# Kernel tuning notes

Hardware: AMD Instinct MI355X
Metric: run time of the kernel (lower is better)

The kernel has to match this reference:

```python
import jax, jax.numpy as jnp
import numpy as np

N_USERS = 100000
N_ITEMS = 50000
N = N_USERS + N_ITEMS
EMB_DIM = 64
N_LAYERS = 3
NNZ = 6400000
BATCH = 4096


def setup_inputs() -> dict:
    key = jax.random.key(0)
    k = jax.random.split(key, 7)
    user_emb = 0.1 * jax.random.normal(k[0], (N_USERS, EMB_DIM), dtype=jnp.float32)
    item_emb = 0.1 * jax.random.normal(k[1], (N_ITEMS, EMB_DIM), dtype=jnp.float32)
    graph_val = jax.random.uniform(k[2], (NNZ,), dtype=jnp.float32) * 0.05
    graph_src = jax.random.randint(k[3], (NNZ,), 0, N, dtype=jnp.int64) if jax.config.jax_enable_x64 else jax.random.randint(k[3], (NNZ,), 0, N).astype(jnp.int32)
    graph_dst = jax.random.randint(k[4], (NNZ,), 0, N).astype(graph_src.dtype)
    users = jax.random.randint(k[5], (BATCH,), 0, N_USERS).astype(graph_src.dtype)
    items = jax.random.randint(k[6], (BATCH,), 0, N_ITEMS).astype(graph_src.dtype)
    return {"user_emb": user_emb, "item_emb": item_emb, "graph_val": graph_val,
            "graph_src": graph_src, "graph_dst": graph_dst, "users": users, "items": items}


def _spmm(val, src, dst, x):
    # y[src] += val * x[dst]  -- sparse (COO) matrix @ dense
    return jax.ops.segment_sum(val[:, None] * x[dst], src, num_segments=N)


def reference(user_emb, item_emb, graph_val, graph_src, graph_dst, users, items):
    all_emb = jnp.concatenate([user_emb, item_emb], axis=0)  # [N, d]
    acc = all_emb  # running sum over layers (fused mean accumulation)
    x = all_emb
    for _ in range(N_LAYERS):
        x = _spmm(graph_val, graph_src, graph_dst, x)
        acc = acc + x
    light_out = acc / (N_LAYERS + 1)
    all_users = light_out[:N_USERS]
    all_items = light_out[N_USERS:]
    scores = jnp.sum(all_users[users] * all_items[items], axis=1)  # [B]
    return scores
```

## Files before the change

### kernel.cpp

```cpp
#include <hip/hip_runtime.h>


constexpr int N_USERS = 100000;
constexpr int N_ITEMS = 50000;
constexpr int N_NODES = N_USERS + N_ITEMS;
constexpr int EMB = 64;
constexpr int NNZ = 6400000;
constexpr int BATCH = 4096;

constexpr int BSHIFT = 9;
constexpr int BWIDTH = 1 << BSHIFT;
constexpr int NB = (N_NODES + BWIDTH - 1) >> BSHIFT;
constexpr int NBPAD = 512;
constexpr int BSTRIDE = 23500;
constexpr int PBSTRIDE = 26624;

constexpr int TILE = 5120;
constexpr int P1_BLOCKS = NNZ / TILE;
constexpr int EPT1 = TILE / 256;
constexpr int IQ_BLOCKS = (N_NODES * 8 + 255) / 256;
constexpr int GI_BLOCKS = (BATCH * 2 * 64) / 256;
constexpr int SBLOCKS  = (N_NODES * 8 + 255) / 256;
constexpr int SELBLOCKS = (BATCH * 2 * 8) / 256;

constexpr float QSCALE = 327680.0f;
constexpr float QINV   = 1.0f / 327680.0f;

__device__ __forceinline__ int   ntl_i32(const int* p)   { return __builtin_nontemporal_load(p); }
__device__ __forceinline__ float ntl_f32(const float* p) { return __builtin_nontemporal_load(p); }

__global__ void gcur_init_kernel(int* __restrict__ gcur) {
    int i = blockIdx.x * blockDim.x + threadIdx.x;
    if (i < NB) gcur[i] = i * BSTRIDE;
}

__device__ __forceinline__ float ubf0(unsigned x) { return (float)(x & 0xffu); }
__device__ __forceinline__ float ubf1(unsigned x) { return (float)((x >> 8) & 0xffu); }
__device__ __forceinline__ float ubf2(unsigned x) { return (float)((x >> 16) & 0xffu); }
__device__ __forceinline__ float ubf3(unsigned x) { return (float)(x >> 24); }

__global__ void fused_build_kernel(const int* __restrict__ src, const int* __restrict__ dst,
                                   const float* __restrict__ val, int* __restrict__ gcur,
                                   unsigned* __restrict__ sx, unsigned short* __restrict__ srow,
                                   const float* __restrict__ ue, const float* __restrict__ ie,
                                   const int* __restrict__ users, const int* __restrict__ items,
                                   unsigned char* __restrict__ x8, float* __restrict__ scl,
                                   float* __restrict__ accb) {
    int bx = blockIdx.x;
    int t = threadIdx.x;
    if (bx < P1_BLOCKS) {
        __shared__ int hist[NBPAD];
        __shared__ int gbase[NBPAD];
        __shared__ int cur[NBPAD];
        __shared__ int sbuf[NBPAD];
        __shared__ int lbase[NBPAD];
        __shared__ uint2 ebuf[TILE];
        int tile = bx * TILE;
        int srcs[EPT1];
        #pragma unroll
        for (int k = 0; k < EPT1; ++k) srcs[k] = ntl_i32(src + tile + t + k * 256);
        for (int i = t; i < NBPAD; i += 256) { hist[i] = 0; cur[i] = 0; }
        __syncthreads();
        #pragma unroll
        for (int k = 0; k < EPT1; ++k) atomicAdd(&hist[srcs[k] >> BSHIFT], 1);
        __syncthreads();
        for (int i = t; i < NB; i += 256) {
            int h = hist[i];
            gbase[i] = (h > 0) ? atomicAdd(&gcur[i], h) : 0;
        }
        for (int i = t; i < NBPAD; i += 256) sbuf[i] = hist[i];
        __syncthreads();
        int* pin = sbuf; int* pout = lbase;
        for (int off = 1; off < NBPAD; off <<= 1) {
            for (int i = t; i < NBPAD; i += 256) {
                int v = pin[i];
                if (i >= off) v += pin[i - off];
                pout[i] = v;
            }
            __syncthreads();
            int* tmp = pin; pin = pout; pout = tmp;
        }
        for (int i = t; i < NBPAD; i += 256) lbase[i] = pin[i] - hist[i];
        __syncthreads();
        #pragma unroll
        for (int k = 0; k < EPT1; ++k) {
            int i = tile + t + k * 256;
            int s = srcs[k];
            int b = s >> BSHIFT;
            int c = atomicAdd(&cur[b], 1);
            int d = ntl_i32(dst + i);
            float v = ntl_f32(val + i);
            unsigned q = (unsigned)(v * QSCALE);
            if (q > 16383u) q = 16383u;
            ebuf[lbase[b] + c] = make_uint2((q << 18) | (unsigned)d, (unsigned)s);
        }
        __syncthreads();
        #pragma unroll
        for (int k = 0; k < EPT1; ++k) {
            int j = t + k * 256;
            uint2 e = ebuf[j];
            int b = (int)(e.y >> BSHIFT);
            unsigned pos = (unsigned)(gbase[b] + (j - lbase[b]));
            if (pos < (unsigned)((b + 1) * BSTRIDE)) {
                sx[pos] = e.x;
                srow[pos] = (unsigned short)(e.y & (BWIDTH - 1));
            }
        }
        return;
    }
    bx -= P1_BLOCKS;
    if (bx < IQ_BLOCKS) {
        int gid = bx * 256 + t;
        int row = gid >> 3;
        if (row >= N_NODES) return;
        int l8 = t & 7;
        const float* srcp = (row < N_USERS) ? (ue + (size_t)row * EMB)
                                            : (ie + (size_t)(row - N_USERS) * EMB);
        const float4* p = (const float4*)(srcp + l8 * 8);
        float4 f0 = p[0], f1 = p[1];
        float v[8] = {f0.x, f0.y, f0.z, f0.w, f1.x, f1.y, f1.z, f1.w};
        float m = 0.f;
        #pragma unroll
        for (int k = 0; k < 8; ++k) m = fmaxf(m, fabsf(v[k]));
        m = fmaxf(m, __shfl_xor(m, 1, 64));
        m = fmaxf(m, __shfl_xor(m, 2, 64));
        m = fmaxf(m, __shfl_xor(m, 4, 64));
        float inv = (m > 0.f) ? 127.f / m : 0.f;
        unsigned w0 = 0, w1 = 0;
        #pragma unroll
        for (int k = 0; k < 4; ++k)
            w0 |= (((unsigned)((int)rintf(v[k] * inv) + 128)) & 0xffu) << (8 * k);
        #pragma unroll
        for (int k = 0; k < 4; ++k)
            w1 |= (((unsigned)((int)rintf(v[4 + k] * inv) + 128)) & 0xffu) << (8 * k);
        *(uint2*)(x8 + (((size_t)row) << 6) + l8 * 8) = make_uint2(w0, w1);
        if (l8 == 0) scl[row] = m * (1.f / 127.f);
        return;
    }
    bx -= IQ_BLOCKS;
    {
        int gid = bx * 256 + t;
        int w = gid >> 6;
        int lane = t & 63;
        if (w >= BATCH * 2) return;
        int b = w >> 1;
        float v;
        if (w & 1) v = ie[(long long)items[b] * EMB + lane];
        else       v = ue[(long long)users[b] * EMB + lane];
        accb[(long long)w * EMB + lane] = v;
    }
}

__global__ void p2_sort_kernel(const int* __restrict__ gcur,
                               const unsigned* __restrict__ sx,
                               const unsigned short* __restrict__ srow,
                               unsigned* __restrict__ epack, unsigned* __restrict__ prow) {
    __shared__ int hist[BWIDTH], sA[BWIDTH], sB[BWIDTH], cur[BWIDTH];
    int b = blockIdx.x;
    int t = threadIdx.x;
    int cnt = gcur[b] - b * BSTRIDE;
    if (cnt > BSTRIDE) cnt = BSTRIDE;
    if (cnt < 0) cnt = 0;
    int sbase = b * BSTRIDE;
    hist[t] = 0;
    __syncthreads();
    for (int j = t; j < cnt; j += 512)
        atomicAdd(&hist[srow[sbase + j]], 1);
    __syncthreads();
    sA[t] = (hist[t] + 7) >> 3;
    __syncthreads();
    int* pin = sA; int* pout = sB;
    for (int off = 1; off < BWIDTH; off <<= 1) {
        int v = pin[t];
        if (t >= off) v += pin[t - off];
        pout[t] = v;
        __syncthreads();
        int* tmp = pin; pin = pout; pout = tmp;
    }
    {
        int c = hist[t];
        int pw = (c + 7) >> 3;
        int ps = pin[t] - pw;
        unsigned poff = (unsigned)(b * PBSTRIDE + 8 * ps);
        int fit = (PBSTRIDE - 8 * ps) >> 3;
        if (fit < 0) fit = 0;
        if (pw > fit) pw = fit;
        if (pw > 15) pw = 15;
        cur[t] = (int)poff;
        int node = (b << BSHIFT) + t;
        if (node < N_NODES) prow[node] = (poff << 4) | (unsigned)pw;
        for (int s = c; s < 8 * pw; ++s) epack[poff + s] = 0;
    }
    __syncthreads();
    unsigned bend = (unsigned)((b + 1) * PBSTRIDE);
    for (int j = t; j < cnt; j += 512) {
        int row = (int)srow[sbase + j];
        unsigned ex = sx[sbase + j];
        int p = atomicAdd(&cur[row], 1);
        if ((unsigned)p < bend) epack[p] = ex;
    }
}

__device__ __forceinline__ void row_gather_q8(unsigned pr, int lane,
                                              const unsigned* __restrict__ epack,
                                              const unsigned char* __restrict__ x8,
                                              const float* __restrict__ scl,
                                              float acc[8]) {
    const int l8 = lane & 7;
    const int qb = lane & 56;
    const unsigned li8 = (unsigned)l8 * 8u;
    float a0 = 0, a1 = 0, a2 = 0, a3 = 0, a4 = 0, a5 = 0, a6 = 0, a7 = 0;
    float b0 = 0, b1 = 0, b2 = 0, b3 = 0, b4 = 0, b5 = 0, b6 = 0, b7 = 0;
    float S = 0.f;
    const unsigned* ep = epack + (pr >> 4);
    int nwin = (int)(pr & 15u);
    if (nwin > 0) {
        unsigned e = ep[l8];
        for (int w = 0; w < nwin; ++w) {
            unsigned en = ep[8 + l8];
            ep += 8;
            unsigned d = e & 0x3FFFFu;
            float v = ((float)(e >> 18) + 0.5f) * QINV;
            float vs = v * scl[d];
            unsigned voff = d << 6;
            #pragma unroll
            for (int t = 0; t < 8; t += 2) {
                unsigned offA = (unsigned)__shfl((int)voff, qb + t, 64);
                unsigned offB = (unsigned)__shfl((int)voff, qb + t + 1, 64);
                float vA = __shfl(vs, qb + t, 64);
                float vB = __shfl(vs, qb + t + 1, 64);
                uint2 pa = *(const uint2*)(x8 + (offA | li8));
                uint2 pb = *(const uint2*)(x8 + (offB | li8));
                a0 += vA * ubf0(pa.x);  a1 += vA * ubf1(pa.x);
                a2 += vA * ubf2(pa.x);  a3 += vA * ubf3(pa.x);
                a4 += vA * ubf0(pa.y);  a5 += vA * ubf1(pa.y);
                a6 += vA * ubf2(pa.y);  a7 += vA * ubf3(pa.y);
                b0 += vB * ubf0(pb.x);  b1 += vB * ubf1(pb.x);
                b2 += vB * ubf2(pb.x);  b3 += vB * ubf3(pb.x);
                b4 += vB * ubf0(pb.y);  b5 += vB * ubf1(pb.y);
                b6 += vB * ubf2(pb.y);  b7 += vB * ubf3(pb.y);
                S += vA + vB;
            }
            e = en;
        }
    }
    float c = 128.f * S;
    acc[0] = a0 + b0 - c; acc[1] = a1 + b1 - c; acc[2] = a2 + b2 - c;
    acc[3] = a3 + b3 - c; acc[4] = a4 + b4 - c; acc[5] = a5 + b5 - c;
    acc[6] = a6 + b6 - c; acc[7] = a7 + b7 - c;
}

__global__ void spmmq_fused_kernel(const unsigned* __restrict__ prow,
                                   const unsigned* __restrict__ epack,
                                   const unsigned char* __restrict__ x8in,
                                   const float* __restrict__ sclin,
                                   unsigned char* __restrict__ y8,
                                   float* __restrict__ sclout,
                                   const int* __restrict__ users,
                                   const int* __restrict__ items,
                                   float* __restrict__ accb) {
    int bx = blockIdx.x;
    int t = threadIdx.x;
    if (bx < SBLOCKS) {
        int gid = bx * 256 + t;
        int row = gid >> 3;
        if (row >= N_NODES) return;
        int lane = t & 63;
        unsigned pr = prow[row];
        float acc[8];
        row_gather_q8(pr, lane, epack, x8in, sclin, acc);
        float m = 0.f;
        #pragma unroll
        for (int k = 0; k < 8; ++k) m = fmaxf(m, fabsf(acc[k]));
        m = fmaxf(m, __shfl_xor(m, 1, 64));
        m = fmaxf(m, __shfl_xor(m, 2, 64));
        m = fmaxf(m, __shfl_xor(m, 4, 64));
        float inv = (m > 0.f) ? 127.f / m : 0.f;
        unsigned w0 = 0, w1 = 0;
        #pragma unroll
        for (int k = 0; k < 4; ++k)
            w0 |= (((unsigned)((int)rintf(acc[k] * inv) + 128)) & 0xffu) << (8 * k);
        #pragma unroll
        for (int k = 0; k < 4; ++k)
            w1 |= (((unsigned)((int)rintf(acc[4 + k] * inv) + 128)) & 0xffu) << (8 * k);
        int l8 = lane & 7;
        *(uint2*)(y8 + (((size_t)row) << 6) + l8 * 8) = make_uint2(w0, w1);
        if (l8 == 0) sclout[row] = m * (1.f / 127.f);
        return;
    }
    bx -= SBLOCKS;
    {
        int gid = bx * 256 + t;
        int w = gid >> 6;
        int lane = t & 63;
        if (w >= BATCH * 2) return;
        int b = w >> 1;
        int node = (w & 1) ? (N_USERS + items[b]) : users[b];
        float s = sclin[node];
        float xv = s * ((float)x8in[(((size_t)node) << 6) + lane] - 128.f);
        accb[(long long)w * EMB + lane] += xv;
    }
}

__global__ void tail_kernel(const unsigned* __restrict__ prow,
                            const unsigned* __restrict__ epack,
                            const unsigned char* __restrict__ x8,
                            const float* __restrict__ scl,
                            const int* __restrict__ users, const int* __restrict__ items,
                            float* __restrict__ accb) {
    int bx = blockIdx.x;
    int t = threadIdx.x;
    if (bx < GI_BLOCKS) {
        int gid = bx * 256 + t;
        int w = gid >> 6;
        int lane = t & 63;
        if (w >= BATCH * 2) return;
        int b = w >> 1;
        int node = (w & 1) ? (N_USERS + items[b]) : users[b];
        float s = scl[node];
        float xv = s * ((float)x8[(((size_t)node) << 6) + lane] - 128.f);
        atomicAdd(&accb[(long long)w * EMB + lane], xv);
        return;
    }
    bx -= GI_BLOCKS;
    {
        int gid = bx * 256 + t;
        int g = gid >> 3;
        if (g >= BATCH * 2) return;
        int lane = t & 63;
        int b = g >> 1;
        int node = (g & 1) ? (N_USERS + items[b]) : users[b];
        float acc[8];
        row_gather_q8(prow[node], lane, epack, x8, scl, acc);
        float* p = accb + ((long long)g << 6) + (lane & 7) * 8;
        #pragma unroll
        for (int k = 0; k < 8; ++k) atomicAdd(p + k, acc[k]);
    }
}

__global__ void score_kernel(const float* __restrict__ accb, float* __restrict__ out) {
    int gid = blockIdx.x * blockDim.x + threadIdx.x;
    int b = gid >> 6;
    int lane = threadIdx.x & 63;
    if (b >= BATCH) return;
    float a = accb[(long long)(2 * b) * EMB + lane];
    float c = accb[(long long)(2 * b + 1) * EMB + lane];
    float p = a * c;
    #pragma unroll
    for (int off = 32; off > 0; off >>= 1) p += __shfl_down(p, off, 64);
    if (lane == 0) out[b] = p * (1.0f / 16.0f);
}

extern "C" void kernel_launch(void* const* d_in, const int* in_sizes, int n_in,
                              void* d_out, int out_size, void* d_ws, size_t ws_size,
                              hipStream_t stream) {
    const float* user_emb  = (const float*)d_in[0];
    const float* item_emb  = (const float*)d_in[1];
    const float* graph_val = (const float*)d_in[2];
    const int*   graph_src = (const int*)d_in[3];
    const int*   graph_dst = (const int*)d_in[4];
    const int*   users     = (const int*)d_in[5];
    const int*   items     = (const int*)d_in[6];
    float* out = (float*)d_out;

    char* base = (char*)d_ws;
    const size_t SX_BYTES   = (size_t)BSTRIDE * NB * 4;
    const size_t SROW_BYTES = (size_t)BSTRIDE * NB * 2;
    const size_t XQBYTES    = (size_t)N_NODES * 64;
    const size_t PB_SLOTS   = (size_t)PBSTRIDE * NB;
    unsigned char*  A8    = (unsigned char*)base;
    unsigned char*  B8    = A8 + XQBYTES;
    unsigned*       sx    = (unsigned*)(base + XQBYTES);
    unsigned short* srow  = (unsigned short*)(base + XQBYTES + SX_BYTES);
    char*           p2end = base + XQBYTES + SX_BYTES + ((SROW_BYTES + 63) & ~(size_t)63);
    unsigned*       epack = (unsigned*)p2end;
    unsigned*       prow  = epack + PB_SLOTS;
    int*            gcur  = (int*)(prow + N_NODES);
    float*          accb  = (float*)(gcur + 512);
    float*          scA   = accb + (size_t)BATCH * 2 * EMB;
    float*          scB   = scA + N_NODES;

    gcur_init_kernel<<<(NB + 255) / 256, 256, 0, stream>>>(gcur);
    fused_build_kernel<<<P1_BLOCKS + IQ_BLOCKS + GI_BLOCKS, 256, 0, stream>>>(
        graph_src, graph_dst, graph_val, gcur, sx, srow,
        user_emb, item_emb, users, items, A8, scA, accb);
    p2_sort_kernel<<<NB, 512, 0, stream>>>(gcur, sx, srow, epack, prow);

    spmmq_fused_kernel<<<SBLOCKS, 256, 0, stream>>>(prow, epack, A8, scA, B8, scB,
                                                    users, items, accb);
    spmmq_fused_kernel<<<SBLOCKS + GI_BLOCKS, 256, 0, stream>>>(prow, epack, B8, scB,
                                                                A8, scA, users, items, accb);
    tail_kernel<<<GI_BLOCKS + SELBLOCKS, 256, 0, stream>>>(prow, epack, A8, scA,
                                                           users, items, accb);
    score_kernel<<<(BATCH * 64) / 256, 256, 0, stream>>>(accb, out);
}
```

Measured before the change: 492.1 us.

## Split each SpMM layer into two column-half passes with fp16 partial sums

Edges are now bucketed per row by whether the destination column is below or above a split point. Each propagation layer runs as two kernels: one gathers only the low-half columns and writes fp16 partial rows, the other gathers the high-half columns, adds the partial, and requantizes to int8. The goal is to halve the randomly gathered embedding working set per pass so it fits better in cache. The cost is an extra fp16 partial write and read per layer, more window padding from splitting rows, and some extra rounding in the partials.

Result: slower. 515.5 us (+4.8%).

```diff
diff --git a/kernel.cpp b/kernel.cpp
--- a/kernel.cpp
+++ b/kernel.cpp
@@ -7,13 +7,15 @@
 constexpr int EMB = 64;
 constexpr int NNZ = 6400000;
 constexpr int BATCH = 4096;
+constexpr int DSPLIT = 75000;
 
 constexpr int BSHIFT = 9;
 constexpr int BWIDTH = 1 << BSHIFT;
 constexpr int NB = (N_NODES + BWIDTH - 1) >> BSHIFT;
 constexpr int NBPAD = 512;
 constexpr int BSTRIDE = 23500;
-constexpr int PBSTRIDE = 26624;
+constexpr int PBSTRIDE = 27648;
+constexpr int PBW = PBSTRIDE / 8;
 
 constexpr int TILE = 5120;
 constexpr int P1_BLOCKS = NNZ / TILE;
@@ -28,6 +30,8 @@
 
 __device__ __forceinline__ int   ntl_i32(const int* p)   { return __builtin_nontemporal_load(p); }
 __device__ __forceinline__ float ntl_f32(const float* p) { return __builtin_nontemporal_load(p); }
+__device__ __forceinline__ unsigned long long ntl_u64(const unsigned long long* p) { return __builtin_nontemporal_load(p); }
+__device__ __forceinline__ void nts_u64(unsigned long long v, unsigned long long* p) { __builtin_nontemporal_store(v, p); }
 
 __global__ void gcur_init_kernel(int* __restrict__ gcur) {
     int i = blockIdx.x * blockDim.x + threadIdx.x;
@@ -92,18 +96,21 @@
             float v = ntl_f32(val + i);
             unsigned q = (unsigned)(v * QSCALE);
             if (q > 16383u) q = 16383u;
-            ebuf[lbase[b] + c] = make_uint2((q << 18) | (unsigned)d, (unsigned)s);
+            unsigned half = (d >= DSPLIT) ? 512u : 0u;
+            ebuf[lbase[b] + c] = make_uint2((q << 18) | (unsigned)d,
+                                            (unsigned)(s & (BWIDTH - 1)) | half |
+                                            ((unsigned)b << 10));
         }
         __syncthreads();
         #pragma unroll
         for (int k = 0; k < EPT1; ++k) {
             int j = t + k * 256;
             uint2 e = ebuf[j];
-            int b = (int)(e.y >> BSHIFT);
+            int b = (int)(e.y >> 10);
             unsigned pos = (unsigned)(gbase[b] + (j - lbase[b]));
             if (pos < (unsigned)((b + 1) * BSTRIDE)) {
                 sx[pos] = e.x;
-                srow[pos] = (unsigned short)(e.y & (BWIDTH - 1));
+                srow[pos] = (unsigned short)(e.y & 1023u);
             }
         }
         return;
@@ -155,54 +162,68 @@
                                const unsigned* __restrict__ sx,
                                const unsigned short* __restrict__ srow,
                                unsigned* __restrict__ epack, unsigned* __restrict__ prow) {
-    __shared__ int hist[BWIDTH], sA[BWIDTH], sB[BWIDTH], cur[BWIDTH];
+    __shared__ int hist[1024], sA[1024], sB[1024], cur[1024];
     int b = blockIdx.x;
     int t = threadIdx.x;
     int cnt = gcur[b] - b * BSTRIDE;
     if (cnt > BSTRIDE) cnt = BSTRIDE;
     if (cnt < 0) cnt = 0;
     int sbase = b * BSTRIDE;
-    hist[t] = 0;
+    hist[t] = 0; hist[t + 512] = 0;
     __syncthreads();
-    for (int j = t; j < cnt; j += 512)
-        atomicAdd(&hist[srow[sbase + j]], 1);
+    for (int j = t; j < cnt; j += 512) {
+        unsigned sr = srow[sbase + j];
+        int key = (int)((sr & 511u) << 1) | (int)(sr >> 9);
+        atomicAdd(&hist[key], 1);
+    }
     __syncthreads();
     sA[t] = (hist[t] + 7) >> 3;
+    sA[t + 512] = (hist[t + 512] + 7) >> 3;
     __syncthreads();
     int* pin = sA; int* pout = sB;
-    for (int off = 1; off < BWIDTH; off <<= 1) {
-        int v = pin[t];
-        if (t >= off) v += pin[t - off];
-        pout[t] = v;
+    for (int off = 1; off < 1024; off <<= 1) {
+        for (int i = t; i < 1024; i += 512) {
+            int v = pin[i];
+            if (i >= off) v += pin[i - off];
+            pout[i] = v;
+        }
         __syncthreads();
         int* tmp = pin; pin = pout; pout = tmp;
     }
     {
-        int c = hist[t];
-        int pw = (c + 7) >> 3;
-        int ps = pin[t] - pw;
-        unsigned poff = (unsigned)(b * PBSTRIDE + 8 * ps);
-        int fit = (PBSTRIDE - 8 * ps) >> 3;
-        if (fit < 0) fit = 0;
-        if (pw > fit) pw = fit;
-        if (pw > 15) pw = 15;
-        cur[t] = (int)poff;
+        int clo = hist[2 * t], chi = hist[2 * t + 1];
+        int nlo = (clo + 7) >> 3, nhi = (chi + 7) >> 3;
+        int ws = pin[2 * t + 1] - nlo - nhi;
+        int fitw = PBW - ws;
+        if (fitw < 0) fitw = 0;
+        if (nlo > fitw) nlo = fitw;
+        if (nlo > 15) nlo = 15;
+        int fitw2 = fitw - nlo;
+        if (nhi > fitw2) nhi = fitw2;
+        if (nhi > 15) nhi = 15;
+        unsigned wsg = (unsigned)(b * PBW + ws);
+        unsigned pofflo = wsg * 8u;
+        unsigned poffhi = pofflo + (unsigned)nlo * 8u;
+        cur[2 * t] = (int)pofflo;
+        cur[2 * t + 1] = (int)poffhi;
         int node = (b << BSHIFT) + t;
-        if (node < N_NODES) prow[node] = (poff << 4) | (unsigned)pw;
-        for (int s = c; s < 8 * pw; ++s) epack[poff + s] = 0;
+        if (node < N_NODES)
+            prow[node] = (wsg << 8) | ((unsigned)nlo << 4) | (unsigned)nhi;
+        for (int s = clo; s < 8 * nlo; ++s) epack[pofflo + s] = 0;
+        for (int s = chi; s < 8 * nhi; ++s) epack[poffhi + s] = 0;
     }
     __syncthreads();
     unsigned bend = (unsigned)((b + 1) * PBSTRIDE);
     for (int j = t; j < cnt; j += 512) {
-        int row = (int)srow[sbase + j];
-        unsigned ex = sx[sbase + j];
-        int p = atomicAdd(&cur[row], 1);
-        if ((unsigned)p < bend) epack[p] = ex;
-    }
-}
-
-__device__ __forceinline__ void row_gather_q8(unsigned pr, int lane,
-                                              const unsigned* __restrict__ epack,
+        unsigned sr = srow[sbase + j];
+        int key = (int)((sr & 511u) << 1) | (int)(sr >> 9);
+        int p = atomicAdd(&cur[key], 1);
+        if ((unsigned)p < bend) epack[p] = sx[sbase + j];
+    }
+}
+
+__device__ __forceinline__ void row_gather_q8(const unsigned* __restrict__ ep, int nwin,
+                                              int lane,
                                               const unsigned char* __restrict__ x8,
                                               const float* __restrict__ scl,
                                               float acc[8]) {
@@ -212,8 +233,6 @@
     float a0 = 0, a1 = 0, a2 = 0, a3 = 0, a4 = 0, a5 = 0, a6 = 0, a7 = 0;
     float b0 = 0, b1 = 0, b2 = 0, b3 = 0, b4 = 0, b5 = 0, b6 = 0, b7 = 0;
     float S = 0.f;
-    const unsigned* ep = epack + (pr >> 4);
-    int nwin = (int)(pr & 15u);
     if (nwin > 0) {
         unsigned e = ep[l8];
         for (int w = 0; w < nwin; ++w) {
@@ -250,15 +269,14 @@
     acc[6] = a6 + b6 - c; acc[7] = a7 + b7 - c;
 }
 
-__global__ void spmmq_fused_kernel(const unsigned* __restrict__ prow,
-                                   const unsigned* __restrict__ epack,
-                                   const unsigned char* __restrict__ x8in,
-                                   const float* __restrict__ sclin,
-                                   unsigned char* __restrict__ y8,
-                                   float* __restrict__ sclout,
-                                   const int* __restrict__ users,
-                                   const int* __restrict__ items,
-                                   float* __restrict__ accb) {
+__global__ void spmmA_kernel(const unsigned* __restrict__ prow,
+                             const unsigned* __restrict__ epack,
+                             const unsigned char* __restrict__ x8in,
+                             const float* __restrict__ sclin,
+                             _Float16* __restrict__ partial,
+                             const int* __restrict__ users,
+                             const int* __restrict__ items,
+                             float* __restrict__ accb) {
     int bx = blockIdx.x;
     int t = threadIdx.x;
     if (bx < SBLOCKS) {
@@ -268,24 +286,15 @@
         int lane = t & 63;
         unsigned pr = prow[row];
         float acc[8];
-        row_gather_q8(pr, lane, epack, x8in, sclin, acc);
-        float m = 0.f;
-        #pragma unroll
-        for (int k = 0; k < 8; ++k) m = fmaxf(m, fabsf(acc[k]));
-        m = fmaxf(m, __shfl_xor(m, 1, 64));
-        m = fmaxf(m, __shfl_xor(m, 2, 64));
-        m = fmaxf(m, __shfl_xor(m, 4, 64));
-        float inv = (m > 0.f) ? 127.f / m : 0.f;
-        unsigned w0 = 0, w1 = 0;
-        #pragma unroll
-        for (int k = 0; k < 4; ++k)
-            w0 |= (((unsigned)((int)rintf(acc[k] * inv) + 128)) & 0xffu) << (8 * k);
-        #pragma unroll
-        for (int k = 0; k < 4; ++k)
-            w1 |= (((unsigned)((int)rintf(acc[4 + k] * inv) + 128)) & 0xffu) << (8 * k);
+        row_gather_q8(epack + (size_t)(pr >> 8) * 8, (int)((pr >> 4) & 15u),
+                      lane, x8in, sclin, acc);
         int l8 = lane & 7;
-        *(uint2*)(y8 + (((size_t)row) << 6) + l8 * 8) = make_uint2(w0, w1);
-        if (l8 == 0) sclout[row] = m * (1.f / 127.f);
+        union { _Float16 h[4]; unsigned long long u; } plo, phi;
+        #pragma unroll
+        for (int k = 0; k < 4; ++k) { plo.h[k] = (_Float16)acc[k]; phi.h[k] = (_Float16)acc[4 + k]; }
+        _Float16* pp = partial + (((size_t)row) << 6) + l8 * 8;
+        nts_u64(plo.u, (unsigned long long*)pp);
+        nts_u64(phi.u, (unsigned long long*)(pp + 4));
         return;
     }
     bx -= SBLOCKS;
@@ -300,6 +309,47 @@
         float xv = s * ((float)x8in[(((size_t)node) << 6) + lane] - 128.f);
         accb[(long long)w * EMB + lane] += xv;
     }
+}
+
+__global__ void spmmB_kernel(const unsigned* __restrict__ prow,
+                             const unsigned* __restrict__ epack,
+                             const unsigned char* __restrict__ x8in,
+                             const float* __restrict__ sclin,
+                             const _Float16* __restrict__ partial,
+                             unsigned char* __restrict__ y8,
+                             float* __restrict__ sclout) {
+    int gid = blockIdx.x * blockDim.x + threadIdx.x;
+    int row = gid >> 3;
+    if (row >= N_NODES) return;
+    int lane = threadIdx.x & 63;
+    unsigned pr = prow[row];
+    unsigned nlo = (pr >> 4) & 15u;
+    float acc[8];
+    row_gather_q8(epack + ((size_t)(pr >> 8) + nlo) * 8, (int)(pr & 15u),
+                  lane, x8in, sclin, acc);
+    int l8 = lane & 7;
+    const _Float16* pp = partial + (((size_t)row) << 6) + l8 * 8;
+    union { unsigned long long u; _Float16 h[4]; } plo, phi;
+    plo.u = ntl_u64((const unsigned long long*)pp);
+    phi.u = ntl_u64((const unsigned long long*)(pp + 4));
+    #pragma unroll
+    for (int k = 0; k < 4; ++k) { acc[k] += (float)plo.h[k]; acc[4 + k] += (float)phi.h[k]; }
+    float m = 0.f;
+    #pragma unroll
+    for (int k = 0; k < 8; ++k) m = fmaxf(m, fabsf(acc[k]));
+    m = fmaxf(m, __shfl_xor(m, 1, 64));
+    m = fmaxf(m, __shfl_xor(m, 2, 64));
+    m = fmaxf(m, __shfl_xor(m, 4, 64));
+    float inv = (m > 0.f) ? 127.f / m : 0.f;
+    unsigned w0 = 0, w1 = 0;
+    #pragma unroll
+    for (int k = 0; k < 4; ++k)
+        w0 |= (((unsigned)((int)rintf(acc[k] * inv) + 128)) & 0xffu) << (8 * k);
+    #pragma unroll
+    for (int k = 0; k < 4; ++k)
+        w1 |= (((unsigned)((int)rintf(acc[4 + k] * inv) + 128)) & 0xffu) << (8 * k);
+    *(uint2*)(y8 + (((size_t)row) << 6) + l8 * 8) = make_uint2(w0, w1);
+    if (l8 == 0) sclout[row] = m * (1.f / 127.f);
 }
 
 __global__ void tail_kernel(const unsigned* __restrict__ prow,
@@ -330,8 +380,10 @@
         int lane = t & 63;
         int b = g >> 1;
         int node = (g & 1) ? (N_USERS + items[b]) : users[b];
+        unsigned pr = prow[node];
+        int ntot = (int)((pr >> 4) & 15u) + (int)(pr & 15u);
         float acc[8];
-        row_gather_q8(prow[node], lane, epack, x8, scl, acc);
+        row_gather_q8(epack + (size_t)(pr >> 8) * 8, ntot, lane, x8, scl, acc);
         float* p = accb + ((long long)g << 6) + (lane & 7) * 8;
         #pragma unroll
         for (int k = 0; k < 8; ++k) atomicAdd(p + k, acc[k]);
@@ -368,17 +420,18 @@
     const size_t SROW_BYTES = (size_t)BSTRIDE * NB * 2;
     const size_t XQBYTES    = (size_t)N_NODES * 64;
     const size_t PB_SLOTS   = (size_t)PBSTRIDE * NB;
-    unsigned char*  A8    = (unsigned char*)base;
-    unsigned char*  B8    = A8 + XQBYTES;
-    unsigned*       sx    = (unsigned*)(base + XQBYTES);
-    unsigned short* srow  = (unsigned short*)(base + XQBYTES + SX_BYTES);
-    char*           p2end = base + XQBYTES + SX_BYTES + ((SROW_BYTES + 63) & ~(size_t)63);
-    unsigned*       epack = (unsigned*)p2end;
-    unsigned*       prow  = epack + PB_SLOTS;
-    int*            gcur  = (int*)(prow + N_NODES);
-    float*          accb  = (float*)(gcur + 512);
-    float*          scA   = accb + (size_t)BATCH * 2 * EMB;
-    float*          scB   = scA + N_NODES;
+    unsigned char*  A8      = (unsigned char*)base;
+    unsigned char*  B8      = A8 + XQBYTES;
+    _Float16*       partial = (_Float16*)(base + 2 * XQBYTES);
+    unsigned*       sx      = (unsigned*)(base + XQBYTES);
+    unsigned short* srow    = (unsigned short*)(base + XQBYTES + SX_BYTES);
+    char*           p2end   = base + XQBYTES + SX_BYTES + ((SROW_BYTES + 63) & ~(size_t)63);
+    unsigned*       epack   = (unsigned*)p2end;
+    unsigned*       prow    = epack + PB_SLOTS;
+    int*            gcur    = (int*)(prow + N_NODES);
+    float*          accb    = (float*)(gcur + 512);
+    float*          scA     = accb + (size_t)BATCH * 2 * EMB;
+    float*          scB     = scA + N_NODES;
 
     gcur_init_kernel<<<(NB + 255) / 256, 256, 0, stream>>>(gcur);
     fused_build_kernel<<<P1_BLOCKS + IQ_BLOCKS + GI_BLOCKS, 256, 0, stream>>>(
@@ -386,10 +439,12 @@
         user_emb, item_emb, users, items, A8, scA, accb);
     p2_sort_kernel<<<NB, 512, 0, stream>>>(gcur, sx, srow, epack, prow);
 
-    spmmq_fused_kernel<<<SBLOCKS, 256, 0, stream>>>(prow, epack, A8, scA, B8, scB,
-                                                    users, items, accb);
-    spmmq_fused_kernel<<<SBLOCKS + GI_BLOCKS, 256, 0, stream>>>(prow, epack, B8, scB,
-                                                                A8, scA, users, items, accb);
+    spmmA_kernel<<<SBLOCKS, 256, 0, stream>>>(prow, epack, A8, scA, partial,
+                                              users, items, accb);
+    spmmB_kernel<<<SBLOCKS, 256, 0, stream>>>(prow, epack, A8, scA, partial, B8, scB);
+    spmmA_kernel<<<SBLOCKS + GI_BLOCKS, 256, 0, stream>>>(prow, epack, B8, scB, partial,
+                                                          users, items, accb);
+    spmmB_kernel<<<SBLOCKS, 256, 0, stream>>>(prow, epack, B8, scB, partial, A8, scA);
     tail_kernel<<<GI_BLOCKS + SELBLOCKS, 256, 0, stream>>>(prow, epack, A8, scA,
                                                            users, items, accb);
     score_kernel<<<(BATCH * 64) / 256, 256, 0, stream>>>(accb, out);
```
